# Performance work log

Measured on AMD Instinct MI355X. Metric: run time of the kernel, lower is better.

Reference implementation:

```python
import jax, jax.numpy as jnp
import numpy as np

B, S, H, E, I, TOPK = 4, 1024, 1024, 8, 2048, 2
SOFT_CAP = 30.0
W_SCALE = 0.02


def setup_inputs() -> dict:
    key = jax.random.key(0)
    k0, k1, k2, k3, k4 = jax.random.split(key, 5)
    return {
        "hidden_states": jax.random.normal(k0, (B, S, H), dtype=jnp.float32),
        "w_gate": jax.random.normal(k1, (E, H), dtype=jnp.float32) * W_SCALE,
        "w1": jax.random.normal(k2, (E, I, H), dtype=jnp.float32) * W_SCALE,
        "w3": jax.random.normal(k3, (E, I, H), dtype=jnp.float32) * W_SCALE,
        "w2": jax.random.normal(k4, (E, H, I), dtype=jnp.float32) * W_SCALE,
        "top_k": TOPK,
    }


def reference(hidden_states, w_gate, w1, w3, w2, top_k):
    orig_shape = hidden_states.shape
    x = hidden_states.reshape(-1, orig_shape[-1])  # [T, H]
    # Router gate + soft cap
    logits = x @ w_gate.T  # [T, E]
    logits = SOFT_CAP * jnp.tanh(logits / SOFT_CAP)
    probs = jax.nn.softmax(logits, axis=-1)
    # top-k routing, renormalize=False -> use softmax probs directly
    top_w, top_i = jax.lax.top_k(probs, top_k)  # [T, k]
    T, nE = probs.shape
    gates = jnp.zeros((T, nE), probs.dtype).at[
        jnp.arange(T)[:, None], top_i
    ].add(top_w)  # [T, E] sparse routing weights
    # Grouped expert GEMMs with gated GELU (GeluAndMul)
    h1 = jnp.einsum('th,eih->tei', x, w1)  # [T, E, I]
    h3 = jnp.einsum('th,eih->tei', x, w3)
    act = jax.nn.gelu(h1, approximate=False) * h3
    y = jnp.einsum('tei,ehi->teh', act, w2)  # [T, E, H]
    out = jnp.einsum('te,teh->th', gates, y)
    return out.reshape(orig_shape)
```

## Files before the change

kernel.cpp:

```cpp
#include <hip/hip_runtime.h>
#include <stdint.h>

#define T_TOK 4096
#define HDIM  1024
#define NEXP  8
#define IDIM  2048
#define BK    64
#define NASSIGN (T_TOK * 2)

typedef short short8 __attribute__((ext_vector_type(8)));
typedef float f32x4 __attribute__((ext_vector_type(4)));

__device__ __forceinline__ unsigned short f32_to_bf16(float f) {
  union { float f; uint32_t u; } v; v.f = f;
  uint32_t r = 0x7FFFu + ((v.u >> 16) & 1u);
  return (unsigned short)((v.u + r) >> 16);
}

__device__ __forceinline__ void gload16(const void* g, void* l) {
  __builtin_amdgcn_global_load_lds(
      (const __attribute__((address_space(1))) uint32_t*)g,
      (__attribute__((address_space(3))) uint32_t*)l, 16, 0, 0);
}

__global__ void cast_w3_kernel(const float* __restrict__ w1,
                               const float* __restrict__ w3,
                               const float* __restrict__ w2,
                               unsigned short* __restrict__ w1b,
                               unsigned short* __restrict__ w3b,
                               unsigned short* __restrict__ w2b, int n8) {
  int i = blockIdx.x * blockDim.x + threadIdx.x;
  if (i >= n8) return;
  const float* src; unsigned short* dst;
  if (blockIdx.y == 0)      { src = w1; dst = w1b; }
  else if (blockIdx.y == 1) { src = w3; dst = w3b; }
  else                      { src = w2; dst = w2b; }
  const float4* s = (const float4*)src + (size_t)i * 2;
  float4 a = s[0], b = s[1];
  short8 o;
  o[0] = f32_to_bf16(a.x); o[1] = f32_to_bf16(a.y);
  o[2] = f32_to_bf16(a.z); o[3] = f32_to_bf16(a.w);
  o[4] = f32_to_bf16(b.x); o[5] = f32_to_bf16(b.y);
  o[6] = f32_to_bf16(b.z); o[7] = f32_to_bf16(b.w);
  ((short8*)dst)[i] = o;
}

__global__ __launch_bounds__(256)
void router_core(const float* __restrict__ x, const float* __restrict__ wg,
                 unsigned short* __restrict__ xb,
                 unsigned char* __restrict__ eids,
                 float* __restrict__ gate_a) {
  __shared__ float wgs[NEXP * HDIM];
  const int tid = threadIdx.x;
#pragma unroll
  for (int i = 0; i < NEXP * HDIM / 4 / 256; ++i)
    ((float4*)wgs)[i * 256 + tid] = ((const float4*)wg)[i * 256 + tid];
  __syncthreads();

  const int wv = tid >> 6, lane = tid & 63;
#pragma unroll
  for (int tt = 0; tt < 2; ++tt) {
    const int t = blockIdx.x * 8 + wv * 2 + tt;
    const float* xr = x + (size_t)t * HDIM;
    float acc0 = 0.f, acc1v = 0.f, acc2 = 0.f, acc3 = 0.f;
    float acc4 = 0.f, acc5 = 0.f, acc6 = 0.f, acc7 = 0.f;
#pragma unroll
    for (int it = 0; it < 4; ++it) {
      const int j = it * 256 + lane * 4;
      const float4 xv = *(const float4*)(xr + j);
      ushort4 u;
      u.x = f32_to_bf16(xv.x); u.y = f32_to_bf16(xv.y);
      u.z = f32_to_bf16(xv.z); u.w = f32_to_bf16(xv.w);
      *(ushort4*)(xb + (size_t)t * HDIM + j) = u;
      const float4 g0 = *(const float4*)(wgs + 0 * HDIM + j);
      const float4 g1 = *(const float4*)(wgs + 1 * HDIM + j);
      const float4 g2 = *(const float4*)(wgs + 2 * HDIM + j);
      const float4 g3 = *(const float4*)(wgs + 3 * HDIM + j);
      const float4 g4 = *(const float4*)(wgs + 4 * HDIM + j);
      const float4 g5 = *(const float4*)(wgs + 5 * HDIM + j);
      const float4 g6 = *(const float4*)(wgs + 6 * HDIM + j);
      const float4 g7 = *(const float4*)(wgs + 7 * HDIM + j);
      acc0 += xv.x * g0.x + xv.y * g0.y + xv.z * g0.z + xv.w * g0.w;
      acc1v += xv.x * g1.x + xv.y * g1.y + xv.z * g1.z + xv.w * g1.w;
      acc2 += xv.x * g2.x + xv.y * g2.y + xv.z * g2.z + xv.w * g2.w;
      acc3 += xv.x * g3.x + xv.y * g3.y + xv.z * g3.z + xv.w * g3.w;
      acc4 += xv.x * g4.x + xv.y * g4.y + xv.z * g4.z + xv.w * g4.w;
      acc5 += xv.x * g5.x + xv.y * g5.y + xv.z * g5.z + xv.w * g5.w;
      acc6 += xv.x * g6.x + xv.y * g6.y + xv.z * g6.z + xv.w * g6.w;
      acc7 += xv.x * g7.x + xv.y * g7.y + xv.z * g7.z + xv.w * g7.w;
    }
    float acc[NEXP] = {acc0, acc1v, acc2, acc3, acc4, acc5, acc6, acc7};
#pragma unroll
    for (int e = 0; e < NEXP; ++e) {
#pragma unroll
      for (int off = 32; off > 0; off >>= 1) acc[e] += __shfl_xor(acc[e], off);
    }
    if (lane == 0) {
      float p[NEXP];
      float mx = -1e30f;
#pragma unroll
      for (int e = 0; e < NEXP; ++e) {
        float l = 30.0f * tanhf(acc[e] * (1.0f / 30.0f));
        p[e] = l;
        mx = fmaxf(mx, l);
      }
      float s = 0.f;
#pragma unroll
      for (int e = 0; e < NEXP; ++e) { p[e] = expf(p[e] - mx); s += p[e]; }
      const float inv = 1.0f / s;
#pragma unroll
      for (int e = 0; e < NEXP; ++e) p[e] *= inv;
      int i0 = 0;
#pragma unroll
      for (int e = 1; e < NEXP; ++e) if (p[e] > p[i0]) i0 = e;
      int i1 = (i0 == 0) ? 1 : 0;
#pragma unroll
      for (int e = 0; e < NEXP; ++e) if (e != i1 && e != i0 && p[e] > p[i1]) i1 = e;
      eids[t * 2]     = (unsigned char)i0;
      gate_a[t * 2]   = p[i0];
      eids[t * 2 + 1] = (unsigned char)i1;
      gate_a[t * 2 + 1] = p[i1];
    }
  }
}

__global__ __launch_bounds__(1024)
void build_lists(const unsigned char* __restrict__ eids,
                 int* __restrict__ counts, int* __restrict__ list) {
  const int e = blockIdx.x;
  const int tid = threadIdx.x;
  const int wid = tid >> 6, lane = tid & 63;
  __shared__ int wave_tot[16];
  __shared__ int running;
  if (tid == 0) running = 0;
  __syncthreads();
#pragma unroll
  for (int c = 0; c < NASSIGN; c += 1024) {
    const int slot = c + tid;
    const bool match = ((int)eids[slot] == e);
    const unsigned long long mask = __ballot(match);
    if (lane == 0) wave_tot[wid] = __popcll(mask);
    __syncthreads();
    int base = running;
    for (int w = 0; w < wid; ++w) base += wave_tot[w];
    if (match) {
      const int pre = __popcll(mask & ((1ull << lane) - 1ull));
      list[e * T_TOK + base + pre] = slot;
    }
    __syncthreads();
    if (tid == 0) {
      int tot = 0;
      for (int w = 0; w < 16; ++w) tot += wave_tot[w];
      running += tot;
    }
    __syncthreads();
  }
  if (tid == 0) counts[e] = running;
}

__global__ __launch_bounds__(512, 2)
void moe_gemm1_fast(const unsigned short* __restrict__ xb,
                    const unsigned short* __restrict__ w1b,
                    const unsigned short* __restrict__ w3b,
                    const int* __restrict__ counts, const int* __restrict__ list,
                    unsigned short* __restrict__ act) {
  const int e = blockIdx.z;
  const int cnt = counts[e];
  const int m0 = blockIdx.y * 256;
  if (m0 >= cnt) return;
  const int n0 = blockIdx.x * 64;

  __shared__ __align__(16) unsigned short As[256 * BK];
  __shared__ __align__(16) unsigned short B1s[64 * BK];
  __shared__ __align__(16) unsigned short B3s[64 * BK];
  __shared__ int entry_l[256];

  const int tid = threadIdx.x;
  if (tid < 256) entry_l[tid] = (m0 + tid < cnt) ? list[e * T_TOK + m0 + tid] : -1;
  __syncthreads();

  const int lane = tid & 63;
  const int l15 = lane & 15;
  const int kg  = lane >> 4;
  const int wid = tid >> 6;
  const int wvu = __builtin_amdgcn_readfirstlane(wid);
  const int wm = wid >> 1, wn = wid & 1;

  const int srow8  = lane >> 3;
  const int schunk = (lane & 7) ^ srow8;

  const unsigned short* aSrc[4];
#pragma unroll
  for (int r = 0; r < 4; ++r) {
    const int row = r * 64 + wid * 8 + srow8;
    const int en = entry_l[row];
    const int tok = (en >= 0) ? (en >> 1) : 0;
    aSrc[r] = xb + (size_t)tok * HDIM + schunk * 8;
  }
  const unsigned short* b1Src = w1b + ((size_t)e * IDIM + n0 + wid * 8 + srow8) * HDIM + schunk * 8;
  const unsigned short* b3Src = w3b + ((size_t)e * IDIM + n0 + wid * 8 + srow8) * HDIM + schunk * 8;

  int aOff[4][2], bOff[2][2];
#pragma unroll
  for (int mf = 0; mf < 4; ++mf)
#pragma unroll
    for (int ks = 0; ks < 2; ++ks) {
      const int row = wm * 64 + mf * 16 + l15;
      aOff[mf][ks] = row * 128 + (((ks * 4 + kg) ^ (row & 7)) * 16);
    }
#pragma unroll
  for (int nf = 0; nf < 2; ++nf)
#pragma unroll
    for (int ks = 0; ks < 2; ++ks) {
      const int row = wn * 32 + nf * 16 + l15;
      bOff[nf][ks] = row * 128 + (((ks * 4 + kg) ^ (row & 7)) * 16);
    }

  f32x4 acc1[4][2], acc3[4][2];
#pragma unroll
  for (int mf = 0; mf < 4; ++mf)
#pragma unroll
    for (int nf = 0; nf < 2; ++nf) {
      acc1[mf][nf] = (f32x4){0.f, 0.f, 0.f, 0.f};
      acc3[mf][nf] = (f32x4){0.f, 0.f, 0.f, 0.f};
    }

  const char* AsB = (const char*)As;
  const char* B1B = (const char*)B1s;
  const char* B3B = (const char*)B3s;

  for (int k0 = 0; k0 < HDIM; k0 += BK) {
#pragma unroll
    for (int r = 0; r < 4; ++r) gload16(aSrc[r], As + r * 4096 + wvu * 512);
    gload16(b1Src, B1s + wvu * 512);
    gload16(b3Src, B3s + wvu * 512);
#pragma unroll
    for (int r = 0; r < 4; ++r) aSrc[r] += BK;
    b1Src += BK; b3Src += BK;
    __syncthreads();

    short8 af[4][2], b1f[2][2], b3f[2][2];
#pragma unroll
    for (int mf = 0; mf < 4; ++mf)
#pragma unroll
      for (int ks = 0; ks < 2; ++ks)
        af[mf][ks] = *(const short8*)(AsB + aOff[mf][ks]);
#pragma unroll
    for (int nf = 0; nf < 2; ++nf)
#pragma unroll
      for (int ks = 0; ks < 2; ++ks) {
        b1f[nf][ks] = *(const short8*)(B1B + bOff[nf][ks]);
        b3f[nf][ks] = *(const short8*)(B3B + bOff[nf][ks]);
      }
#pragma unroll
    for (int mf = 0; mf < 4; ++mf)
#pragma unroll
      for (int nf = 0; nf < 2; ++nf)
#pragma unroll
        for (int ks = 0; ks < 2; ++ks) {
          acc1[mf][nf] = __builtin_amdgcn_mfma_f32_16x16x32_bf16(af[mf][ks], b1f[nf][ks], acc1[mf][nf], 0, 0, 0);
          acc3[mf][nf] = __builtin_amdgcn_mfma_f32_16x16x32_bf16(af[mf][ks], b3f[nf][ks], acc3[mf][nf], 0, 0, 0);
        }
    __syncthreads();
  }

#pragma unroll
  for (int mf = 0; mf < 4; ++mf) {
#pragma unroll
    for (int i = 0; i < 4; ++i) {
      const int r = wm * 64 + mf * 16 + kg * 4 + i;
      const int en = entry_l[r];
      if (en < 0) continue;
      unsigned short* arow = act + (size_t)en * IDIM + n0 + wn * 32;
#pragma unroll
      for (int nf = 0; nf < 2; ++nf) {
        const float h1 = acc1[mf][nf][i];
        const float h3 = acc3[mf][nf][i];
        const float g = 0.5f * h1 * (1.0f + erff(h1 * 0.70710678118f));
        arow[nf * 16 + l15] = f32_to_bf16(g * h3);
      }
    }
  }
}

__global__ __launch_bounds__(512, 2)
void moe_gemm2_fast(const unsigned short* __restrict__ act,
                    const unsigned short* __restrict__ w2b,
                    const int* __restrict__ counts, const int* __restrict__ list,
                    const float* __restrict__ gate_a,
                    float* __restrict__ ybuf) {
  const int e = blockIdx.z;
  const int cnt = counts[e];
  const int m0 = blockIdx.y * 256;
  if (m0 >= cnt) return;
  const int n0 = blockIdx.x * 128;

  __shared__ __align__(16) unsigned short As[256 * BK];
  __shared__ __align__(16) unsigned short Bs[128 * BK];
  __shared__ int entry_l[256];

  const int tid = threadIdx.x;
  if (tid < 256) entry_l[tid] = (m0 + tid < cnt) ? list[e * T_TOK + m0 + tid] : -1;
  __syncthreads();

  const int lane = tid & 63;
  const int l15 = lane & 15;
  const int kg  = lane >> 4;
  const int wid = tid >> 6;
  const int wvu = __builtin_amdgcn_readfirstlane(wid);
  const int wm = wid >> 1, wn = wid & 1;

  const int srow8  = lane >> 3;
  const int schunk = (lane & 7) ^ srow8;

  const unsigned short* aSrc[4];
#pragma unroll
  for (int r = 0; r < 4; ++r) {
    const int row = r * 64 + wid * 8 + srow8;
    const int en = entry_l[row];
    const int arow = (en >= 0) ? en : 0;
    aSrc[r] = act + (size_t)arow * IDIM + schunk * 8;
  }
  const unsigned short* bSrc[2];
#pragma unroll
  for (int r = 0; r < 2; ++r) {
    const int row = r * 64 + wid * 8 + srow8;
    bSrc[r] = w2b + ((size_t)e * HDIM + n0 + row) * IDIM + schunk * 8;
  }

  int aOff[4][2], bOff[4][2];
#pragma unroll
  for (int mf = 0; mf < 4; ++mf)
#pragma unroll
    for (int ks = 0; ks < 2; ++ks) {
      const int row = wm * 64 + mf * 16 + l15;
      aOff[mf][ks] = row * 128 + (((ks * 4 + kg) ^ (row & 7)) * 16);
    }
#pragma unroll
  for (int nf = 0; nf < 4; ++nf)
#pragma unroll
    for (int ks = 0; ks < 2; ++ks) {
      const int row = wn * 64 + nf * 16 + l15;
      bOff[nf][ks] = row * 128 + (((ks * 4 + kg) ^ (row & 7)) * 16);
    }

  f32x4 acc[4][4];
#pragma unroll
  for (int mf = 0; mf < 4; ++mf)
#pragma unroll
    for (int nf = 0; nf < 4; ++nf) acc[mf][nf] = (f32x4){0.f, 0.f, 0.f, 0.f};

  const char* AsB = (const char*)As;
  const char* BsB = (const char*)Bs;

  for (int k0 = 0; k0 < IDIM; k0 += BK) {
#pragma unroll
    for (int r = 0; r < 4; ++r) gload16(aSrc[r], As + r * 4096 + wvu * 512);
#pragma unroll
    for (int r = 0; r < 2; ++r) gload16(bSrc[r], Bs + r * 4096 + wvu * 512);
#pragma unroll
    for (int r = 0; r < 4; ++r) aSrc[r] += BK;
#pragma unroll
    for (int r = 0; r < 2; ++r) bSrc[r] += BK;
    __syncthreads();

    short8 af[4][2], bf[4][2];
#pragma unroll
    for (int mf = 0; mf < 4; ++mf)
#pragma unroll
      for (int ks = 0; ks < 2; ++ks)
        af[mf][ks] = *(const short8*)(AsB + aOff[mf][ks]);
#pragma unroll
    for (int nf = 0; nf < 4; ++nf)
#pragma unroll
      for (int ks = 0; ks < 2; ++ks)
        bf[nf][ks] = *(const short8*)(BsB + bOff[nf][ks]);
#pragma unroll
    for (int mf = 0; mf < 4; ++mf)
#pragma unroll
      for (int nf = 0; nf < 4; ++nf)
#pragma unroll
        for (int ks = 0; ks < 2; ++ks)
          acc[mf][nf] = __builtin_amdgcn_mfma_f32_16x16x32_bf16(af[mf][ks], bf[nf][ks], acc[mf][nf], 0, 0, 0);
    __syncthreads();
  }

#pragma unroll
  for (int mf = 0; mf < 4; ++mf) {
#pragma unroll
    for (int i = 0; i < 4; ++i) {
      const int r = wm * 64 + mf * 16 + kg * 4 + i;
      const int en = entry_l[r];
      if (en < 0) continue;
      const float gate = gate_a[en];
      float* yrow = ybuf + (size_t)en * HDIM + n0 + wn * 64;
#pragma unroll
      for (int nf = 0; nf < 4; ++nf)
        yrow[nf * 16 + l15] = acc[mf][nf][i] * gate;
    }
  }
}

__global__ __launch_bounds__(256)
void combine_kernel(const float* __restrict__ ybuf, float* __restrict__ out) {
  const int i = blockIdx.x * 256 + threadIdx.x;
  const int t  = i >> 8;
  const int j4 = i & 255;
  const float4 a = ((const float4*)(ybuf + (size_t)(2 * t) * HDIM))[j4];
  const float4 b = ((const float4*)(ybuf + (size_t)(2 * t + 1) * HDIM))[j4];
  float4 o;
  o.x = a.x + b.x; o.y = a.y + b.y; o.z = a.z + b.z; o.w = a.w + b.w;
  ((float4*)out)[i] = o;
}

#define LSTRIDE 40

__global__ __launch_bounds__(256, 2)
void moe_gemm1_fb(const unsigned short* __restrict__ xb,
                  const float* __restrict__ w1, const float* __restrict__ w3,
                  const int* __restrict__ counts, const int* __restrict__ list,
                  unsigned short* __restrict__ act) {
  const int e = blockIdx.z;
  const int cnt = counts[e];
  const int m0 = blockIdx.y * 128;
  if (m0 >= cnt) return;
  const int n0 = blockIdx.x * 64;

  __shared__ short As[128 * LSTRIDE];
  __shared__ short B1s[64 * LSTRIDE];
  __shared__ short B3s[64 * LSTRIDE];
  __shared__ int entry_l[128];

  const int tid = threadIdx.x;
  if (tid < 128) entry_l[tid] = (m0 + tid < cnt) ? list[e * T_TOK + m0 + tid] : -1;
  __syncthreads();

  const int lane = tid & 63;
  const int l15 = lane & 15;
  const int kg = lane >> 4;
  const int wv = tid >> 6;
  const int wm = wv >> 1, wn = wv & 1;

  f32x4 acc1[4][2], acc3[4][2];
#pragma unroll
  for (int mf = 0; mf < 4; ++mf)
#pragma unroll
    for (int nf = 0; nf < 2; ++nf) {
      acc1[mf][nf] = (f32x4){0.f, 0.f, 0.f, 0.f};
      acc3[mf][nf] = (f32x4){0.f, 0.f, 0.f, 0.f};
    }

  const int srow = tid >> 2;
  const int scol = (tid & 3) << 3;

  const float* w1base = w1 + ((size_t)e * IDIM + n0) * HDIM;
  const float* w3base = w3 + ((size_t)e * IDIM + n0) * HDIM;

  for (int k0 = 0; k0 < HDIM; k0 += 32) {
#pragma unroll
    for (int it = 0; it < 2; ++it) {
      const int r = srow + it * 64;
      const int en = entry_l[r];
      uint4 v = {0u, 0u, 0u, 0u};
      if (en >= 0)
        v = *(const uint4*)(xb + ((size_t)(en >> 1) * HDIM + k0 + scol));
      *(uint4*)(&As[r * LSTRIDE + scol]) = v;
    }
    {
      const float* p1 = w1base + (size_t)srow * HDIM + k0 + scol;
      float4 a0 = *(const float4*)(p1);
      float4 a1 = *(const float4*)(p1 + 4);
      short8 sb;
      sb[0] = f32_to_bf16(a0.x); sb[1] = f32_to_bf16(a0.y);
      sb[2] = f32_to_bf16(a0.z); sb[3] = f32_to_bf16(a0.w);
      sb[4] = f32_to_bf16(a1.x); sb[5] = f32_to_bf16(a1.y);
      sb[6] = f32_to_bf16(a1.z); sb[7] = f32_to_bf16(a1.w);
      *(short8*)(&B1s[srow * LSTRIDE + scol]) = sb;
      const float* p3 = w3base + (size_t)srow * HDIM + k0 + scol;
      float4 c0 = *(const float4*)(p3);
      float4 c1 = *(const float4*)(p3 + 4);
      sb[0] = f32_to_bf16(c0.x); sb[1] = f32_to_bf16(c0.y);
      sb[2] = f32_to_bf16(c0.z); sb[3] = f32_to_bf16(c0.w);
      sb[4] = f32_to_bf16(c1.x); sb[5] = f32_to_bf16(c1.y);
      sb[6] = f32_to_bf16(c1.z); sb[7] = f32_to_bf16(c1.w);
      *(short8*)(&B3s[srow * LSTRIDE + scol]) = sb;
    }
    __syncthreads();
    short8 af[4], b1f[2], b3f[2];
#pragma unroll
    for (int mf = 0; mf < 4; ++mf)
      af[mf] = *(const short8*)(&As[(wm * 64 + mf * 16 + l15) * LSTRIDE + kg * 8]);
#pragma unroll
    for (int nf = 0; nf < 2; ++nf) {
      b1f[nf] = *(const short8*)(&B1s[(wn * 32 + nf * 16 + l15) * LSTRIDE + kg * 8]);
      b3f[nf] = *(const short8*)(&B3s[(wn * 32 + nf * 16 + l15) * LSTRIDE + kg * 8]);
    }
#pragma unroll
    for (int mf = 0; mf < 4; ++mf)
#pragma unroll
      for (int nf = 0; nf < 2; ++nf) {
        acc1[mf][nf] = __builtin_amdgcn_mfma_f32_16x16x32_bf16(af[mf], b1f[nf], acc1[mf][nf], 0, 0, 0);
        acc3[mf][nf] = __builtin_amdgcn_mfma_f32_16x16x32_bf16(af[mf], b3f[nf], acc3[mf][nf], 0, 0, 0);
      }
    __syncthreads();
  }

#pragma unroll
  for (int mf = 0; mf < 4; ++mf) {
#pragma unroll
    for (int i = 0; i < 4; ++i) {
      const int r = wm * 64 + mf * 16 + kg * 4 + i;
      const int en = entry_l[r];
      if (en < 0) continue;
      unsigned short* arow = act + (size_t)en * IDIM + n0 + wn * 32;
#pragma unroll
      for (int nf = 0; nf < 2; ++nf) {
        const float h1 = acc1[mf][nf][i];
        const float h3 = acc3[mf][nf][i];
        const float g = 0.5f * h1 * (1.0f + erff(h1 * 0.70710678118f));
        arow[nf * 16 + l15] = f32_to_bf16(g * h3);
      }
    }
  }
}

__global__ __launch_bounds__(256, 2)
void moe_gemm2_fb(const unsigned short* __restrict__ act,
                  const float* __restrict__ w2,
                  const int* __restrict__ counts, const int* __restrict__ list,
                  const float* __restrict__ gate_a,
                  float* __restrict__ out) {
  const int e = blockIdx.z;
  const int cnt = counts[e];
  const int m0 = blockIdx.y * 128;
  if (m0 >= cnt) return;
  const int n0 = blockIdx.x * 64;

  __shared__ short As[128 * LSTRIDE];
  __shared__ short Bs[64 * LSTRIDE];
  __shared__ int entry_l[128];

  const int tid = threadIdx.x;
  if (tid < 128) entry_l[tid] = (m0 + tid < cnt) ? list[e * T_TOK + m0 + tid] : -1;
  __syncthreads();

  const int lane = tid & 63;
  const int l15 = lane & 15;
  const int kg = lane >> 4;
  const int wv = tid >> 6;
  const int wm = wv >> 1, wn = wv & 1;

  f32x4 acc[4][2];
#pragma unroll
  for (int mf = 0; mf < 4; ++mf)
#pragma unroll
    for (int nf = 0; nf < 2; ++nf) acc[mf][nf] = (f32x4){0.f, 0.f, 0.f, 0.f};

  const int srow = tid >> 2;
  const int scol = (tid & 3) << 3;

  const float* w2b2 = w2 + ((size_t)e * HDIM + n0) * IDIM;

  for (int k0 = 0; k0 < IDIM; k0 += 32) {
#pragma unroll
    for (int it = 0; it < 2; ++it) {
      const int r = srow + it * 64;
      const int en = entry_l[r];
      uint4 v = {0u, 0u, 0u, 0u};
      if (en >= 0)
        v = *(const uint4*)(act + ((size_t)en * IDIM + k0 + scol));
      *(uint4*)(&As[r * LSTRIDE + scol]) = v;
    }
    {
      const float* p2 = w2b2 + (size_t)srow * IDIM + k0 + scol;
      float4 a0 = *(const float4*)(p2);
      float4 a1 = *(const float4*)(p2 + 4);
      short8 sb;
      sb[0] = f32_to_bf16(a0.x); sb[1] = f32_to_bf16(a0.y);
      sb[2] = f32_to_bf16(a0.z); sb[3] = f32_to_bf16(a0.w);
      sb[4] = f32_to_bf16(a1.x); sb[5] = f32_to_bf16(a1.y);
      sb[6] = f32_to_bf16(a1.z); sb[7] = f32_to_bf16(a1.w);
      *(short8*)(&Bs[srow * LSTRIDE + scol]) = sb;
    }
    __syncthreads();
    short8 af[4], bf[2];
#pragma unroll
    for (int mf = 0; mf < 4; ++mf)
      af[mf] = *(const short8*)(&As[(wm * 64 + mf * 16 + l15) * LSTRIDE + kg * 8]);
#pragma unroll
    for (int nf = 0; nf < 2; ++nf)
      bf[nf] = *(const short8*)(&Bs[(wn * 32 + nf * 16 + l15) * LSTRIDE + kg * 8]);
#pragma unroll
    for (int mf = 0; mf < 4; ++mf)
#pragma unroll
      for (int nf = 0; nf < 2; ++nf)
        acc[mf][nf] = __builtin_amdgcn_mfma_f32_16x16x32_bf16(af[mf], bf[nf], acc[mf][nf], 0, 0, 0);
    __syncthreads();
  }

#pragma unroll
  for (int mf = 0; mf < 4; ++mf) {
#pragma unroll
    for (int i = 0; i < 4; ++i) {
      const int r = wm * 64 + mf * 16 + kg * 4 + i;
      const int en = entry_l[r];
      if (en < 0) continue;
      const float gate = gate_a[en];
      float* orow = out + (size_t)(en >> 1) * HDIM + n0 + wn * 32;
#pragma unroll
      for (int nf = 0; nf < 2; ++nf)
        atomicAdd(&orow[nf * 16 + l15], acc[mf][nf][i] * gate);
    }
  }
}

extern "C" void kernel_launch(void* const* d_in, const int* in_sizes, int n_in,
                              void* d_out, int out_size, void* d_ws, size_t ws_size,
                              hipStream_t stream) {
  const float* x  = (const float*)d_in[0];
  const float* wg = (const float*)d_in[1];
  const float* w1 = (const float*)d_in[2];
  const float* w3 = (const float*)d_in[3];
  const float* w2 = (const float*)d_in[4];
  float* out = (float*)d_out;

  char* ws = (char*)d_ws;
  int*            counts = (int*)ws;
  int*            list   = (int*)(ws + 1024);
  float*          gate_a = (float*)(ws + 132096);
  unsigned char*  eids   = (unsigned char*)(ws + 165888);
  unsigned short* xb     = (unsigned short*)(ws + 262144);
  const size_t OFF_ACT = 262144 + (size_t)T_TOK * HDIM * 2;
  unsigned short* act    = (unsigned short*)(ws + OFF_ACT);
  const size_t WELEMS = (size_t)NEXP * IDIM * HDIM;
  const size_t OFF_W1B = OFF_ACT + (size_t)2 * T_TOK * IDIM * 2;
  const size_t OFF_W3B = OFF_W1B + WELEMS * 2;
  const size_t OFF_W2B = OFF_W3B + WELEMS * 2;
  const size_t WS_NEED = OFF_W2B + WELEMS * 2;

  router_core<<<T_TOK / 8, 256, 0, stream>>>(x, wg, xb, eids, gate_a);
  build_lists<<<NEXP, 1024, 0, stream>>>(eids, counts, list);

  if (ws_size >= WS_NEED) {
    unsigned short* w1b = (unsigned short*)(ws + OFF_W1B);
    unsigned short* w3b = (unsigned short*)(ws + OFF_W3B);
    unsigned short* w2b = (unsigned short*)(ws + OFF_W2B);
    float* ybuf = (float*)(ws + OFF_W1B);
    const int n8 = (int)(WELEMS / 8);
    cast_w3_kernel<<<dim3((n8 + 255) / 256, 3), 256, 0, stream>>>(w1, w3, w2, w1b, w3b, w2b, n8);
    moe_gemm1_fast<<<dim3(IDIM / 64, T_TOK / 256, NEXP), 512, 0, stream>>>(xb, w1b, w3b, counts, list, act);
    moe_gemm2_fast<<<dim3(HDIM / 128, T_TOK / 256, NEXP), 512, 0, stream>>>(act, w2b, counts, list, gate_a, ybuf);
    combine_kernel<<<T_TOK * HDIM / 4 / 256, 256, 0, stream>>>(ybuf, out);
  } else {
    hipMemsetAsync(d_out, 0, (size_t)out_size * sizeof(float), stream);
    moe_gemm1_fb<<<dim3(IDIM / 64, T_TOK / 128, NEXP), 256, 0, stream>>>(xb, w1, w3, counts, list, act);
    moe_gemm2_fb<<<dim3(HDIM / 64, T_TOK / 128, NEXP), 256, 0, stream>>>(act, w2, counts, list, gate_a, out);
  }
}
```

Baseline: 231.2 us.

## Double-buffer LDS tiles in both MoE GEMM kernels to overlap loads with MFMA

Both expert GEMM kernels now keep two LDS buffers per operand. The next K-tile's global-to-LDS loads are issued before the current tile is computed, using manual vmcnt/lgkmcnt waits, raw s_barrier calls with sched_barrier fences, and raised wave priority around the MFMA block. This is meant to hide global memory latency behind matrix math. It doubles LDS use per block, which may reduce occupancy below the two blocks per CU the launch bounds target. The hand-tuned waitcnt values must also match the number of outstanding loads.

```diff
diff --git a/kernel.cpp b/kernel.cpp
--- a/kernel.cpp
+++ b/kernel.cpp
@@ -170,9 +170,9 @@
   if (m0 >= cnt) return;
   const int n0 = blockIdx.x * 64;
 
-  __shared__ __align__(16) unsigned short As[256 * BK];
-  __shared__ __align__(16) unsigned short B1s[64 * BK];
-  __shared__ __align__(16) unsigned short B3s[64 * BK];
+  __shared__ __align__(16) unsigned short As[2][256 * BK];
+  __shared__ __align__(16) unsigned short B1s[2][64 * BK];
+  __shared__ __align__(16) unsigned short B3s[2][64 * BK];
   __shared__ int entry_l[256];
 
   const int tid = threadIdx.x;
@@ -225,44 +225,84 @@
       acc3[mf][nf] = (f32x4){0.f, 0.f, 0.f, 0.f};
     }
 
-  const char* AsB = (const char*)As;
-  const char* B1B = (const char*)B1s;
-  const char* B3B = (const char*)B3s;
-
-  for (int k0 = 0; k0 < HDIM; k0 += BK) {
-#pragma unroll
-    for (int r = 0; r < 4; ++r) gload16(aSrc[r], As + r * 4096 + wvu * 512);
-    gload16(b1Src, B1s + wvu * 512);
-    gload16(b3Src, B3s + wvu * 512);
-#pragma unroll
-    for (int r = 0; r < 4; ++r) aSrc[r] += BK;
-    b1Src += BK; b3Src += BK;
-    __syncthreads();
-
-    short8 af[4][2], b1f[2][2], b3f[2][2];
-#pragma unroll
-    for (int mf = 0; mf < 4; ++mf)
-#pragma unroll
-      for (int ks = 0; ks < 2; ++ks)
-        af[mf][ks] = *(const short8*)(AsB + aOff[mf][ks]);
-#pragma unroll
-    for (int nf = 0; nf < 2; ++nf)
-#pragma unroll
-      for (int ks = 0; ks < 2; ++ks) {
-        b1f[nf][ks] = *(const short8*)(B1B + bOff[nf][ks]);
-        b3f[nf][ks] = *(const short8*)(B3B + bOff[nf][ks]);
+#define STAGE1(b)                                                         \
+  {                                                                       \
+    _Pragma("unroll")                                                     \
+    for (int r = 0; r < 4; ++r)                                           \
+      gload16(aSrc[r], &As[b][0] + r * 4096 + wvu * 512);                 \
+    gload16(b1Src, &B1s[b][0] + wvu * 512);                               \
+    gload16(b3Src, &B3s[b][0] + wvu * 512);                               \
+    _Pragma("unroll")                                                     \
+    for (int r = 0; r < 4; ++r) aSrc[r] += BK;                            \
+    b1Src += BK; b3Src += BK;                                             \
+  }
+
+#define FRAGS1(cur)                                                       \
+  const char* AsB = (const char*)&As[cur][0];                             \
+  const char* B1B = (const char*)&B1s[cur][0];                            \
+  const char* B3B = (const char*)&B3s[cur][0];                            \
+  short8 af[4][2], b1f[2][2], b3f[2][2];                                  \
+  _Pragma("unroll")                                                       \
+  for (int mf = 0; mf < 4; ++mf)                                          \
+    _Pragma("unroll")                                                     \
+    for (int ks = 0; ks < 2; ++ks)                                        \
+      af[mf][ks] = *(const short8*)(AsB + aOff[mf][ks]);                  \
+  _Pragma("unroll")                                                       \
+  for (int nf = 0; nf < 2; ++nf)                                          \
+    _Pragma("unroll")                                                     \
+    for (int ks = 0; ks < 2; ++ks) {                                      \
+      b1f[nf][ks] = *(const short8*)(B1B + bOff[nf][ks]);                 \
+      b3f[nf][ks] = *(const short8*)(B3B + bOff[nf][ks]);                 \
+    }
+
+#define MFMA1                                                             \
+  _Pragma("unroll")                                                       \
+  for (int mf = 0; mf < 4; ++mf)                                          \
+    _Pragma("unroll")                                                     \
+    for (int nf = 0; nf < 2; ++nf)                                        \
+      _Pragma("unroll")                                                   \
+      for (int ks = 0; ks < 2; ++ks) {                                    \
+        acc1[mf][nf] = __builtin_amdgcn_mfma_f32_16x16x32_bf16(           \
+            af[mf][ks], b1f[nf][ks], acc1[mf][nf], 0, 0, 0);              \
+        acc3[mf][nf] = __builtin_amdgcn_mfma_f32_16x16x32_bf16(           \
+            af[mf][ks], b3f[nf][ks], acc3[mf][nf], 0, 0, 0);              \
       }
-#pragma unroll
-    for (int mf = 0; mf < 4; ++mf)
-#pragma unroll
-      for (int nf = 0; nf < 2; ++nf)
-#pragma unroll
-        for (int ks = 0; ks < 2; ++ks) {
-          acc1[mf][nf] = __builtin_amdgcn_mfma_f32_16x16x32_bf16(af[mf][ks], b1f[nf][ks], acc1[mf][nf], 0, 0, 0);
-          acc3[mf][nf] = __builtin_amdgcn_mfma_f32_16x16x32_bf16(af[mf][ks], b3f[nf][ks], acc3[mf][nf], 0, 0, 0);
-        }
-    __syncthreads();
-  }
+
+  STAGE1(0);
+#pragma unroll
+  for (int t = 0; t < (HDIM / BK) - 1; ++t) {
+    const int cur = t & 1;
+    STAGE1(cur ^ 1);
+    asm volatile("s_waitcnt vmcnt(6)" ::: "memory");
+    __builtin_amdgcn_sched_barrier(0);
+    __builtin_amdgcn_s_barrier();
+    __builtin_amdgcn_sched_barrier(0);
+    {
+      FRAGS1(cur)
+      asm volatile("s_waitcnt lgkmcnt(0)" ::: "memory");
+      __builtin_amdgcn_sched_barrier(0);
+      __builtin_amdgcn_s_barrier();
+      __builtin_amdgcn_s_setprio(1);
+      MFMA1
+      __builtin_amdgcn_s_setprio(0);
+    }
+  }
+  {
+    const int cur = ((HDIM / BK) - 1) & 1;
+    asm volatile("s_waitcnt vmcnt(0)" ::: "memory");
+    __builtin_amdgcn_sched_barrier(0);
+    __builtin_amdgcn_s_barrier();
+    __builtin_amdgcn_sched_barrier(0);
+    {
+      FRAGS1(cur)
+      asm volatile("s_waitcnt lgkmcnt(0)" ::: "memory");
+      __builtin_amdgcn_sched_barrier(0);
+      MFMA1
+    }
+  }
+#undef STAGE1
+#undef FRAGS1
+#undef MFMA1
 
 #pragma unroll
   for (int mf = 0; mf < 4; ++mf) {
@@ -295,8 +335,8 @@
   if (m0 >= cnt) return;
   const int n0 = blockIdx.x * 128;
 
-  __shared__ __align__(16) unsigned short As[256 * BK];
-  __shared__ __align__(16) unsigned short Bs[128 * BK];
+  __shared__ __align__(16) unsigned short As[2][256 * BK];
+  __shared__ __align__(16) unsigned short Bs[2][128 * BK];
   __shared__ int entry_l[256];
 
   const int tid = threadIdx.x;
@@ -350,40 +390,80 @@
 #pragma unroll
     for (int nf = 0; nf < 4; ++nf) acc[mf][nf] = (f32x4){0.f, 0.f, 0.f, 0.f};
 
-  const char* AsB = (const char*)As;
-  const char* BsB = (const char*)Bs;
-
-  for (int k0 = 0; k0 < IDIM; k0 += BK) {
-#pragma unroll
-    for (int r = 0; r < 4; ++r) gload16(aSrc[r], As + r * 4096 + wvu * 512);
-#pragma unroll
-    for (int r = 0; r < 2; ++r) gload16(bSrc[r], Bs + r * 4096 + wvu * 512);
-#pragma unroll
-    for (int r = 0; r < 4; ++r) aSrc[r] += BK;
-#pragma unroll
-    for (int r = 0; r < 2; ++r) bSrc[r] += BK;
-    __syncthreads();
-
-    short8 af[4][2], bf[4][2];
-#pragma unroll
-    for (int mf = 0; mf < 4; ++mf)
-#pragma unroll
-      for (int ks = 0; ks < 2; ++ks)
-        af[mf][ks] = *(const short8*)(AsB + aOff[mf][ks]);
-#pragma unroll
-    for (int nf = 0; nf < 4; ++nf)
-#pragma unroll
-      for (int ks = 0; ks < 2; ++ks)
-        bf[nf][ks] = *(const short8*)(BsB + bOff[nf][ks]);
-#pragma unroll
-    for (int mf = 0; mf < 4; ++mf)
-#pragma unroll
-      for (int nf = 0; nf < 4; ++nf)
-#pragma unroll
-        for (int ks = 0; ks < 2; ++ks)
-          acc[mf][nf] = __builtin_amdgcn_mfma_f32_16x16x32_bf16(af[mf][ks], bf[nf][ks], acc[mf][nf], 0, 0, 0);
-    __syncthreads();
-  }
+#define STAGE2(b)                                                         \
+  {                                                                       \
+    _Pragma("unroll")                                                     \
+    for (int r = 0; r < 4; ++r)                                           \
+      gload16(aSrc[r], &As[b][0] + r * 4096 + wvu * 512);                 \
+    _Pragma("unroll")                                                     \
+    for (int r = 0; r < 2; ++r)                                           \
+      gload16(bSrc[r], &Bs[b][0] + r * 4096 + wvu * 512);                 \
+    _Pragma("unroll")                                                     \
+    for (int r = 0; r < 4; ++r) aSrc[r] += BK;                            \
+    _Pragma("unroll")                                                     \
+    for (int r = 0; r < 2; ++r) bSrc[r] += BK;                            \
+  }
+
+#define FRAGS2(cur)                                                       \
+  const char* AsB = (const char*)&As[cur][0];                             \
+  const char* BsB = (const char*)&Bs[cur][0];                             \
+  short8 af[4][2], bf[4][2];                                              \
+  _Pragma("unroll")                                                       \
+  for (int mf = 0; mf < 4; ++mf)                                          \
+    _Pragma("unroll")                                                     \
+    for (int ks = 0; ks < 2; ++ks)                                        \
+      af[mf][ks] = *(const short8*)(AsB + aOff[mf][ks]);                  \
+  _Pragma("unroll")                                                       \
+  for (int nf = 0; nf < 4; ++nf)                                          \
+    _Pragma("unroll")                                                     \
+    for (int ks = 0; ks < 2; ++ks)                                        \
+      bf[nf][ks] = *(const short8*)(BsB + bOff[nf][ks]);
+
+#define MFMA2                                                             \
+  _Pragma("unroll")                                                       \
+  for (int mf = 0; mf < 4; ++mf)                                          \
+    _Pragma("unroll")                                                     \
+    for (int nf = 0; nf < 4; ++nf)                                        \
+      _Pragma("unroll")                                                   \
+      for (int ks = 0; ks < 2; ++ks)                                      \
+        acc[mf][nf] = __builtin_amdgcn_mfma_f32_16x16x32_bf16(            \
+            af[mf][ks], bf[nf][ks], acc[mf][nf], 0, 0, 0);
+
+  STAGE2(0);
+#pragma unroll
+  for (int t = 0; t < (IDIM / BK) - 1; ++t) {
+    const int cur = t & 1;
+    STAGE2(cur ^ 1);
+    asm volatile("s_waitcnt vmcnt(6)" ::: "memory");
+    __builtin_amdgcn_sched_barrier(0);
+    __builtin_amdgcn_s_barrier();
+    __builtin_amdgcn_sched_barrier(0);
+    {
+      FRAGS2(cur)
+      asm volatile("s_waitcnt lgkmcnt(0)" ::: "memory");
+      __builtin_amdgcn_sched_barrier(0);
+      __builtin_amdgcn_s_barrier();
+      __builtin_amdgcn_s_setprio(1);
+      MFMA2
+      __builtin_amdgcn_s_setprio(0);
+    }
+  }
+  {
+    const int cur = ((IDIM / BK) - 1) & 1;
+    asm volatile("s_waitcnt vmcnt(0)" ::: "memory");
+    __builtin_amdgcn_sched_barrier(0);
+    __builtin_amdgcn_s_barrier();
+    __builtin_amdgcn_sched_barrier(0);
+    {
+      FRAGS2(cur)
+      asm volatile("s_waitcnt lgkmcnt(0)" ::: "memory");
+      __builtin_amdgcn_sched_barrier(0);
+      MFMA2
+    }
+  }
+#undef STAGE2
+#undef FRAGS2
+#undef MFMA2
 
 #pragma unroll
   for (int mf = 0; mf < 4; ++mf) {
```

Result: slower. 287.0 us (+24.1%).
